# Kernel optimization log

Measured on AMD Instinct MI355X. Metric: run time of the kernel, lower is better.

## Reference

```python
import jax, jax.numpy as jnp
import numpy as np

G = 512        # graphs in batch
N_PER = 256    # nodes per graph (equal-size graphs)
D = 128        # embed_dim
E_PER = 4096   # edges per graph
KEEP = 0.5
K = int(np.ceil(KEEP * N_PER))  # 128 nodes kept per graph (PyG topk: ceil(ratio*n))
N = G * N_PER
E = G * E_PER


def setup_inputs() -> dict:
    key = jax.random.key(0)
    k1, k2, k3, k4, k5 = jax.random.split(key, 5)
    x = jax.random.normal(k1, (N, D), jnp.float32)
    offs = (jnp.arange(G, dtype=jnp.int32) * N_PER)[:, None]
    src = jax.random.randint(k2, (G, E_PER), 0, N_PER, dtype=jnp.int32) + offs
    dst = jax.random.randint(k3, (G, E_PER), 0, N_PER, dtype=jnp.int32) + offs
    edge_index = jnp.stack([src.reshape(-1), dst.reshape(-1)], axis=0)  # [2, E], within-graph edges
    graph_indicator = jnp.repeat(jnp.arange(G, dtype=jnp.int32), N_PER)  # [N]
    gcn_w = jax.random.normal(k4, (D, 1), jnp.float32) / np.sqrt(D)
    gcn_b = jnp.zeros((1,), jnp.float32)
    lin_w = jax.random.normal(k5, (2 * D, D), jnp.float32) / np.sqrt(2 * D)
    lin_b = jnp.zeros((D,), jnp.float32)
    return {"input_feature": x, "graph_indicator": graph_indicator, "edge_index": edge_index,
            "gcn_w": gcn_w, "gcn_b": gcn_b, "lin_w": lin_w, "lin_b": lin_b}


def gcn_conv(x, edge_index, w, b):
    # PyG GCNConv: add self-loops, symmetric normalization, aggregate at target (edge_index[1]).
    n = x.shape[0]
    loop = jnp.arange(n, dtype=edge_index.dtype)
    row = jnp.concatenate([edge_index[0], loop])  # source
    col = jnp.concatenate([edge_index[1], loop])  # target
    deg = jax.ops.segment_sum(jnp.ones_like(col, dtype=x.dtype), col, num_segments=n)
    dinv = jax.lax.rsqrt(deg)  # deg >= 1 due to self-loops
    norm = dinv[row] * dinv[col]            # [E+N]
    xw = x @ w                              # [N, out]
    msg = xw[row] * norm[:, None]           # gather + scale
    agg = jax.ops.segment_sum(msg, col, num_segments=n)
    return agg + b


def reference(input_feature, graph_indicator, edge_index, gcn_w, gcn_b, lin_w, lin_b):
    # SAGPool: attention scores via GCNConv(d -> 1)
    score = gcn_conv(input_feature, edge_index, gcn_w, gcn_b).squeeze(-1)  # [N]
    # per-graph top-k mask (equal-size graphs -> reshape)
    s = score.reshape(G, N_PER)
    _, idx = jax.lax.top_k(s, K)                                          # [G, K]
    mask = jnp.zeros((G, N_PER), bool).at[jnp.arange(G)[:, None], idx].set(True)
    # gated features of kept nodes: x[mask] * tanh(score[mask])
    feat = (input_feature * jnp.tanh(score)[:, None]).reshape(G, N_PER, D)
    m = mask[..., None]
    # global mean/max pool over kept nodes per graph (exactly K kept per graph)
    mean = jnp.sum(jnp.where(m, feat, 0.0), axis=1) / K                   # [G, D]
    mx = jnp.max(jnp.where(m, feat, -jnp.inf), axis=1)                    # [G, D]
    readout = jnp.concatenate([mean, mx], axis=1)                         # [G, 2D]
    return readout @ lin_w + lin_b                                        # [G, D]
```

## Files before the change

kernel.cpp:

```cpp
#include <hip/hip_runtime.h>
#include <math.h>

#define NG   512
#define NPER 256
#define DD   128
#define EPER 4096
#define KK   128
#define NT   1024
#define NW   16

#define SFX_SCALE 4194304.0f
#define SFX_INV   2.384185791015625e-07f

#define BAR() asm volatile("s_waitcnt lgkmcnt(0)\ns_barrier" ::: "memory")

__global__ __launch_bounds__(NT, 8) void sag_fused(
    const float* __restrict__ x,
    const int*   __restrict__ esrc,
    const int*   __restrict__ edst,
    const float* __restrict__ gcn_w,
    const float* __restrict__ gcn_b,
    const float* __restrict__ lin_w,
    const float* __restrict__ lin_b,
    float* __restrict__ out)
{
  const int g    = blockIdx.x;
  const int tid  = threadIdx.x;
  const int lane = tid & 63;
  const int wave = tid >> 6;
  const int j    = lane & 15;
  const int sub  = lane >> 4;
  const int slot = wave * 4 + sub;

  __shared__ int    sDeg[NPER];
  __shared__ int    sRank[NPER];
  __shared__ int    sXWi[NPER];
  __shared__ __align__(16) int   sFx[NPER];
  __shared__ float  sXW[NPER];
  __shared__ float  sDinv[NPER];
  __shared__ __align__(16) float sScore[NPER];
  __shared__ float2 sGF[NPER];
  __shared__ float  sPoolS[NW][DD];
  __shared__ float  sPoolM[NW][DD];
  __shared__ float2 sR2[DD];
  float* sR = (float*)sR2;

  const int4* es4 = (const int4*)(esrc + (size_t)g * EPER);
  const int4* ed4 = (const int4*)(edst + (size_t)g * EPER);
  int4 da = ed4[tid];
  int4 sa = es4[tid];

  float4 wa = ((const float4*)gcn_w)[j];
  float4 wb = ((const float4*)gcn_w)[16 + j];

  const float4* xg4 = (const float4*)(x + (size_t)g * NPER * DD);
  const int colbase = slot * 32 + j;
  float4 q0[4], q1[4];
  #pragma unroll
  for (int r = 0; r < 4; ++r) {
    q0[r] = xg4[r * 2048 + colbase];
    q1[r] = xg4[r * 2048 + colbase + 16];
  }

  if (tid < NPER) { sDeg[tid] = 1; sRank[tid] = 0; }
  BAR();

  atomicAdd(&sDeg[da.x & 255], 1);
  atomicAdd(&sDeg[da.y & 255], 1);
  atomicAdd(&sDeg[da.z & 255], 1);
  atomicAdd(&sDeg[da.w & 255], 1);

  #pragma unroll
  for (int r = 0; r < 4; ++r) {
    float acc = q0[r].x*wa.x + q0[r].y*wa.y + q0[r].z*wa.z + q0[r].w*wa.w
              + q1[r].x*wb.x + q1[r].y*wb.y + q1[r].z*wb.z + q1[r].w*wb.w;
    acc += __shfl_xor(acc, 1);
    acc += __shfl_xor(acc, 2);
    acc += __shfl_xor(acc, 4);
    acc += __shfl_xor(acc, 8);
    if (j == 0) sXW[r * 64 + slot] = acc;
  }
  BAR();

  if (tid < NPER) {
    float dv = 1.0f / sqrtf((float)sDeg[tid]);
    int   xi = __float2int_rn(sXW[tid] * dv * SFX_SCALE);
    sDinv[tid] = dv;
    sXWi[tid]  = xi;
    sFx[tid]   = xi;
  }
  BAR();

  {
    int v0 = sXWi[sa.x & 255];
    int v1 = sXWi[sa.y & 255];
    int v2 = sXWi[sa.z & 255];
    int v3 = sXWi[sa.w & 255];
    atomicAdd(&sFx[da.x & 255], v0);
    atomicAdd(&sFx[da.y & 255], v1);
    atomicAdd(&sFx[da.z & 255], v2);
    atomicAdd(&sFx[da.w & 255], v3);
  }
  BAR();

  if (tid < NPER) sScore[tid] = sDinv[tid] * ((float)sFx[tid] * SFX_INV);
  BAR();

  {
    const float4* sScore4 = (const float4*)sScore;
    int node = tid & 255;
    int seg  = tid >> 8;
    float s_i = sScore[node];
    int base = seg * 16;
    int part = 0;
    #pragma unroll 8
    for (int t = 0; t < 16; ++t) {
      float4 v = sScore4[base + t];
      int jj = (base + t) * 4;
      part += (v.x > s_i) || (v.x == s_i && (jj + 0) < node);
      part += (v.y > s_i) || (v.y == s_i && (jj + 1) < node);
      part += (v.z > s_i) || (v.z == s_i && (jj + 2) < node);
      part += (v.w > s_i) || (v.w == s_i && (jj + 3) < node);
    }
    atomicAdd(&sRank[node], part);
  }
  BAR();

  if (tid < NPER) {
    bool kp = sRank[tid] < KK;
    float gate = tanhf(sScore[tid] + gcn_b[0]);
    sGF[tid] = make_float2(kp ? gate : 0.0f, kp ? 0.0f : INFINITY);
  }
  BAR();

  float su0=0,su1=0,su2=0,su3=0,su4=0,su5=0,su6=0,su7=0;
  float mx0=-INFINITY,mx1=-INFINITY,mx2=-INFINITY,mx3=-INFINITY;
  float mx4=-INFINITY,mx5=-INFINITY,mx6=-INFINITY,mx7=-INFINITY;
  #pragma unroll
  for (int r = 0; r < 4; ++r) {
    float2 gf = sGF[r * 64 + slot];
    float g1 = gf.x, fb = gf.y;
    float a;
    a = q0[r].x * g1; su0 += a; mx0 = fmaxf(mx0, a - fb);
    a = q0[r].y * g1; su1 += a; mx1 = fmaxf(mx1, a - fb);
    a = q0[r].z * g1; su2 += a; mx2 = fmaxf(mx2, a - fb);
    a = q0[r].w * g1; su3 += a; mx3 = fmaxf(mx3, a - fb);
    a = q1[r].x * g1; su4 += a; mx4 = fmaxf(mx4, a - fb);
    a = q1[r].y * g1; su5 += a; mx5 = fmaxf(mx5, a - fb);
    a = q1[r].z * g1; su6 += a; mx6 = fmaxf(mx6, a - fb);
    a = q1[r].w * g1; su7 += a; mx7 = fmaxf(mx7, a - fb);
  }
  #define RED_S(v) v += __shfl_xor(v,16); v += __shfl_xor(v,32);
  #define RED_M(v) v = fmaxf(v,__shfl_xor(v,16)); v = fmaxf(v,__shfl_xor(v,32));
  RED_S(su0) RED_S(su1) RED_S(su2) RED_S(su3)
  RED_S(su4) RED_S(su5) RED_S(su6) RED_S(su7)
  RED_M(mx0) RED_M(mx1) RED_M(mx2) RED_M(mx3)
  RED_M(mx4) RED_M(mx5) RED_M(mx6) RED_M(mx7)
  if (sub == 0) {
    ((float4*)&sPoolS[wave][4 * j])[0]      = make_float4(su0, su1, su2, su3);
    ((float4*)&sPoolS[wave][64 + 4 * j])[0] = make_float4(su4, su5, su6, su7);
    ((float4*)&sPoolM[wave][4 * j])[0]      = make_float4(mx0, mx1, mx2, mx3);
    ((float4*)&sPoolM[wave][64 + 4 * j])[0] = make_float4(mx4, mx5, mx6, mx7);
  }
  BAR();

  if (tid < DD) {
    float s = 0.f;
    #pragma unroll
    for (int w = 0; w < NW; ++w) s += sPoolS[w][tid];
    sR[tid] = s * (1.0f / KK);
  } else if (tid < 2 * DD) {
    int d = tid - DD;
    float m = -INFINITY;
    #pragma unroll
    for (int w = 0; w < NW; ++w) m = fmaxf(m, sPoolM[w][d]);
    sR[tid] = m;
  }
  BAR();

  const float2* lw2 = (const float2*)lin_w;
  float a0 = 0.f, a1 = 0.f;
  #pragma unroll
  for (int t = 0; t < 8; ++t) {
    int k2 = wave * 8 + t;
    float2 rv = sR2[k2];
    float2 p0 = lw2[(2 * k2) * 64 + lane];
    float2 p1 = lw2[(2 * k2 + 1) * 64 + lane];
    a0 += rv.x * p0.x + rv.y * p1.x;
    a1 += rv.x * p0.y + rv.y * p1.y;
  }
  float2* sP2 = (float2*)sPoolS;
  sP2[wave * 64 + lane] = make_float2(a0, a1);
  BAR();
  if (wave == 0) {
    float2 a = sP2[lane];
    #pragma unroll
    for (int w = 1; w < NW; ++w) { float2 p = sP2[w * 64 + lane]; a.x += p.x; a.y += p.y; }
    float2 bb = ((const float2*)lin_b)[lane];
    a.x += bb.x; a.y += bb.y;
    ((float2*)out)[(size_t)g * 64 + lane] = a;
  }
}

extern "C" void kernel_launch(void* const* d_in, const int* in_sizes, int n_in,
                              void* d_out, int out_size, void* d_ws, size_t ws_size,
                              hipStream_t stream) {
  const float* x  = (const float*)d_in[0];
  const int*   ei = (const int*)d_in[2];
  const float* gw = (const float*)d_in[3];
  const float* gb = (const float*)d_in[4];
  const float* lw = (const float*)d_in[5];
  const float* lb = (const float*)d_in[6];
  float* out = (float*)d_out;
  const int E = in_sizes[2] / 2;
  sag_fused<<<NG, NT, 0, stream>>>(x, ei, ei + E, gw, gb, lw, lb, out);
}
```

Before: 119.0 us.

## Process two graphs per workgroup and re-read node features for pooling

Each 1024-thread block now handles two graphs, doubling per-block shared-memory arrays and the register-held edge and feature tiles, and the grid shrinks to half as many blocks. The features are loaded once for the score matvec and loaded again from global memory (likely L2-resident) for the pooling phase, so the first copy does not have to stay live across all the barriers. The aim is to amortise the barrier chain and the lin_w reads over two graphs and give each thread more independent memory work. The costs are more registers per thread, lower occupancy (launch bounds drop to 4), half as many blocks to fill the GPU, and a second read of x.

```diff
diff --git a/kernel.cpp b/kernel.cpp
--- a/kernel.cpp
+++ b/kernel.cpp
@@ -7,14 +7,13 @@
 #define EPER 4096
 #define KK   128
 #define NT   1024
-#define NW   16
 
 #define SFX_SCALE 4194304.0f
 #define SFX_INV   2.384185791015625e-07f
 
 #define BAR() asm volatile("s_waitcnt lgkmcnt(0)\ns_barrier" ::: "memory")
 
-__global__ __launch_bounds__(NT, 8) void sag_fused(
+__global__ __launch_bounds__(NT, 4) void sag_fused2(
     const float* __restrict__ x,
     const int*   __restrict__ esrc,
     const int*   __restrict__ edst,
@@ -24,7 +23,8 @@
     const float* __restrict__ lin_b,
     float* __restrict__ out)
 {
-  const int g    = blockIdx.x;
+  const int g0   = blockIdx.x * 2;
+  const int g1x  = g0 + 1;
   const int tid  = threadIdx.x;
   const int lane = tid & 63;
   const int wave = tid >> 6;
@@ -32,173 +32,204 @@
   const int sub  = lane >> 4;
   const int slot = wave * 4 + sub;
 
-  __shared__ int    sDeg[NPER];
-  __shared__ int    sRank[NPER];
-  __shared__ int    sXWi[NPER];
-  __shared__ __align__(16) int   sFx[NPER];
-  __shared__ float  sXW[NPER];
-  __shared__ float  sDinv[NPER];
-  __shared__ __align__(16) float sScore[NPER];
-  __shared__ float2 sGF[NPER];
-  __shared__ float  sPoolS[NW][DD];
-  __shared__ float  sPoolM[NW][DD];
-  __shared__ float2 sR2[DD];
-  float* sR = (float*)sR2;
-
-  const int4* es4 = (const int4*)(esrc + (size_t)g * EPER);
-  const int4* ed4 = (const int4*)(edst + (size_t)g * EPER);
-  int4 da = ed4[tid];
-  int4 sa = es4[tid];
+  __shared__ int    sDeg [2][NPER];
+  __shared__ int    sRank[2][NPER];
+  __shared__ int    sXWi [2][NPER];
+  __shared__ __align__(16) int   sFx[2][NPER];
+  __shared__ float  sXW  [2][NPER];
+  __shared__ float  sDinv[2][NPER];
+  __shared__ __align__(16) float sScore[2][NPER];
+  __shared__ float2 sGF  [2][NPER];
+  __shared__ float  sPoolS[2][16][DD];
+  __shared__ float  sPoolM[2][16][DD];
+  __shared__ float2 sR2  [2][DD];
+
+  const int4* es0 = (const int4*)(esrc + (size_t)g0  * EPER);
+  const int4* ed0 = (const int4*)(edst + (size_t)g0  * EPER);
+  const int4* es1 = (const int4*)(esrc + (size_t)g1x * EPER);
+  const int4* ed1 = (const int4*)(edst + (size_t)g1x * EPER);
+  int4 da0 = ed0[tid], da1 = ed1[tid];
+  int4 sa0 = es0[tid], sa1 = es1[tid];
 
   float4 wa = ((const float4*)gcn_w)[j];
   float4 wb = ((const float4*)gcn_w)[16 + j];
 
-  const float4* xg4 = (const float4*)(x + (size_t)g * NPER * DD);
+  const float4* x0 = (const float4*)(x + (size_t)g0  * NPER * DD);
+  const float4* x1 = (const float4*)(x + (size_t)g1x * NPER * DD);
   const int colbase = slot * 32 + j;
-  float4 q0[4], q1[4];
+
+  float4 qa0[4], qb0[4], qa1[4], qb1[4];
   #pragma unroll
   for (int r = 0; r < 4; ++r) {
-    q0[r] = xg4[r * 2048 + colbase];
-    q1[r] = xg4[r * 2048 + colbase + 16];
-  }
-
-  if (tid < NPER) { sDeg[tid] = 1; sRank[tid] = 0; }
-  BAR();
-
-  atomicAdd(&sDeg[da.x & 255], 1);
-  atomicAdd(&sDeg[da.y & 255], 1);
-  atomicAdd(&sDeg[da.z & 255], 1);
-  atomicAdd(&sDeg[da.w & 255], 1);
+    qa0[r] = x0[r * 2048 + colbase];  qb0[r] = x0[r * 2048 + colbase + 16];
+    qa1[r] = x1[r * 2048 + colbase];  qb1[r] = x1[r * 2048 + colbase + 16];
+  }
+
+  if (tid < 2 * NPER) { ((int*)sDeg)[tid] = 1; ((int*)sRank)[tid] = 0; }
+  BAR();
+
+  atomicAdd(&sDeg[0][da0.x & 255], 1); atomicAdd(&sDeg[1][da1.x & 255], 1);
+  atomicAdd(&sDeg[0][da0.y & 255], 1); atomicAdd(&sDeg[1][da1.y & 255], 1);
+  atomicAdd(&sDeg[0][da0.z & 255], 1); atomicAdd(&sDeg[1][da1.z & 255], 1);
+  atomicAdd(&sDeg[0][da0.w & 255], 1); atomicAdd(&sDeg[1][da1.w & 255], 1);
 
   #pragma unroll
   for (int r = 0; r < 4; ++r) {
-    float acc = q0[r].x*wa.x + q0[r].y*wa.y + q0[r].z*wa.z + q0[r].w*wa.w
-              + q1[r].x*wb.x + q1[r].y*wb.y + q1[r].z*wb.z + q1[r].w*wb.w;
-    acc += __shfl_xor(acc, 1);
-    acc += __shfl_xor(acc, 2);
-    acc += __shfl_xor(acc, 4);
-    acc += __shfl_xor(acc, 8);
-    if (j == 0) sXW[r * 64 + slot] = acc;
-  }
-  BAR();
-
-  if (tid < NPER) {
-    float dv = 1.0f / sqrtf((float)sDeg[tid]);
-    int   xi = __float2int_rn(sXW[tid] * dv * SFX_SCALE);
-    sDinv[tid] = dv;
-    sXWi[tid]  = xi;
-    sFx[tid]   = xi;
+    float a0 = qa0[r].x*wa.x + qa0[r].y*wa.y + qa0[r].z*wa.z + qa0[r].w*wa.w
+             + qb0[r].x*wb.x + qb0[r].y*wb.y + qb0[r].z*wb.z + qb0[r].w*wb.w;
+    float a1 = qa1[r].x*wa.x + qa1[r].y*wa.y + qa1[r].z*wa.z + qa1[r].w*wa.w
+             + qb1[r].x*wb.x + qb1[r].y*wb.y + qb1[r].z*wb.z + qb1[r].w*wb.w;
+    a0 += __shfl_xor(a0, 1);  a1 += __shfl_xor(a1, 1);
+    a0 += __shfl_xor(a0, 2);  a1 += __shfl_xor(a1, 2);
+    a0 += __shfl_xor(a0, 4);  a1 += __shfl_xor(a1, 4);
+    a0 += __shfl_xor(a0, 8);  a1 += __shfl_xor(a1, 8);
+    if (j == 0) { sXW[0][r * 64 + slot] = a0; sXW[1][r * 64 + slot] = a1; }
+  }
+  BAR();
+
+  float4 ua0[4], ub0[4], ua1[4], ub1[4];
+  #pragma unroll
+  for (int r = 0; r < 4; ++r) {
+    ua0[r] = x0[r * 2048 + colbase];  ub0[r] = x0[r * 2048 + colbase + 16];
+    ua1[r] = x1[r * 2048 + colbase];  ub1[r] = x1[r * 2048 + colbase + 16];
+  }
+
+  if (tid < 2 * NPER) {
+    float dv = 1.0f / sqrtf((float)((int*)sDeg)[tid]);
+    int   xi = __float2int_rn(((float*)sXW)[tid] * dv * SFX_SCALE);
+    ((float*)sDinv)[tid] = dv;
+    ((int*)sXWi)[tid]    = xi;
+    ((int*)sFx)[tid]     = xi;
   }
   BAR();
 
   {
-    int v0 = sXWi[sa.x & 255];
-    int v1 = sXWi[sa.y & 255];
-    int v2 = sXWi[sa.z & 255];
-    int v3 = sXWi[sa.w & 255];
-    atomicAdd(&sFx[da.x & 255], v0);
-    atomicAdd(&sFx[da.y & 255], v1);
-    atomicAdd(&sFx[da.z & 255], v2);
-    atomicAdd(&sFx[da.w & 255], v3);
-  }
-  BAR();
-
-  if (tid < NPER) sScore[tid] = sDinv[tid] * ((float)sFx[tid] * SFX_INV);
+    int v0 = sXWi[0][sa0.x & 255], w0 = sXWi[1][sa1.x & 255];
+    int v1 = sXWi[0][sa0.y & 255], w1 = sXWi[1][sa1.y & 255];
+    int v2 = sXWi[0][sa0.z & 255], w2 = sXWi[1][sa1.z & 255];
+    int v3 = sXWi[0][sa0.w & 255], w3 = sXWi[1][sa1.w & 255];
+    atomicAdd(&sFx[0][da0.x & 255], v0); atomicAdd(&sFx[1][da1.x & 255], w0);
+    atomicAdd(&sFx[0][da0.y & 255], v1); atomicAdd(&sFx[1][da1.y & 255], w1);
+    atomicAdd(&sFx[0][da0.z & 255], v2); atomicAdd(&sFx[1][da1.z & 255], w2);
+    atomicAdd(&sFx[0][da0.w & 255], v3); atomicAdd(&sFx[1][da1.w & 255], w3);
+  }
+  BAR();
+
+  if (tid < 2 * NPER)
+    ((float*)sScore)[tid] = ((float*)sDinv)[tid] * ((float)((int*)sFx)[tid] * SFX_INV);
   BAR();
 
   {
-    const float4* sScore4 = (const float4*)sScore;
+    int G    = tid >> 9;
     int node = tid & 255;
-    int seg  = tid >> 8;
-    float s_i = sScore[node];
-    int base = seg * 16;
+    int seg  = (tid >> 8) & 1;
+    const float4* S4 = (const float4*)sScore[G];
+    float s_i = sScore[G][node];
+    int base = seg * 32;
     int part = 0;
     #pragma unroll 8
-    for (int t = 0; t < 16; ++t) {
-      float4 v = sScore4[base + t];
+    for (int t = 0; t < 32; ++t) {
+      float4 v = S4[base + t];
       int jj = (base + t) * 4;
       part += (v.x > s_i) || (v.x == s_i && (jj + 0) < node);
       part += (v.y > s_i) || (v.y == s_i && (jj + 1) < node);
       part += (v.z > s_i) || (v.z == s_i && (jj + 2) < node);
       part += (v.w > s_i) || (v.w == s_i && (jj + 3) < node);
     }
-    atomicAdd(&sRank[node], part);
-  }
-  BAR();
-
-  if (tid < NPER) {
-    bool kp = sRank[tid] < KK;
-    float gate = tanhf(sScore[tid] + gcn_b[0]);
-    sGF[tid] = make_float2(kp ? gate : 0.0f, kp ? 0.0f : INFINITY);
-  }
-  BAR();
-
-  float su0=0,su1=0,su2=0,su3=0,su4=0,su5=0,su6=0,su7=0;
-  float mx0=-INFINITY,mx1=-INFINITY,mx2=-INFINITY,mx3=-INFINITY;
-  float mx4=-INFINITY,mx5=-INFINITY,mx6=-INFINITY,mx7=-INFINITY;
-  #pragma unroll
-  for (int r = 0; r < 4; ++r) {
-    float2 gf = sGF[r * 64 + slot];
-    float g1 = gf.x, fb = gf.y;
-    float a;
-    a = q0[r].x * g1; su0 += a; mx0 = fmaxf(mx0, a - fb);
-    a = q0[r].y * g1; su1 += a; mx1 = fmaxf(mx1, a - fb);
-    a = q0[r].z * g1; su2 += a; mx2 = fmaxf(mx2, a - fb);
-    a = q0[r].w * g1; su3 += a; mx3 = fmaxf(mx3, a - fb);
-    a = q1[r].x * g1; su4 += a; mx4 = fmaxf(mx4, a - fb);
-    a = q1[r].y * g1; su5 += a; mx5 = fmaxf(mx5, a - fb);
-    a = q1[r].z * g1; su6 += a; mx6 = fmaxf(mx6, a - fb);
-    a = q1[r].w * g1; su7 += a; mx7 = fmaxf(mx7, a - fb);
-  }
+    atomicAdd(&sRank[G][node], part);
+  }
+  BAR();
+
+  if (tid < 2 * NPER) {
+    bool kp = ((int*)sRank)[tid] < KK;
+    float gate = tanhf(((float*)sScore)[tid] + gcn_b[0]);
+    ((float2*)sGF)[tid] = make_float2(kp ? gate : 0.0f, kp ? 0.0f : INFINITY);
+  }
+  BAR();
+
   #define RED_S(v) v += __shfl_xor(v,16); v += __shfl_xor(v,32);
   #define RED_M(v) v = fmaxf(v,__shfl_xor(v,16)); v = fmaxf(v,__shfl_xor(v,32));
-  RED_S(su0) RED_S(su1) RED_S(su2) RED_S(su3)
-  RED_S(su4) RED_S(su5) RED_S(su6) RED_S(su7)
-  RED_M(mx0) RED_M(mx1) RED_M(mx2) RED_M(mx3)
-  RED_M(mx4) RED_M(mx5) RED_M(mx6) RED_M(mx7)
-  if (sub == 0) {
-    ((float4*)&sPoolS[wave][4 * j])[0]      = make_float4(su0, su1, su2, su3);
-    ((float4*)&sPoolS[wave][64 + 4 * j])[0] = make_float4(su4, su5, su6, su7);
-    ((float4*)&sPoolM[wave][4 * j])[0]      = make_float4(mx0, mx1, mx2, mx3);
-    ((float4*)&sPoolM[wave][64 + 4 * j])[0] = make_float4(mx4, mx5, mx6, mx7);
-  }
-  BAR();
-
-  if (tid < DD) {
-    float s = 0.f;
+  #define POOL_ONE(G, UA, UB)                                               \
+  {                                                                         \
+    float su0=0,su1=0,su2=0,su3=0,su4=0,su5=0,su6=0,su7=0;                  \
+    float mx0=-INFINITY,mx1=-INFINITY,mx2=-INFINITY,mx3=-INFINITY;          \
+    float mx4=-INFINITY,mx5=-INFINITY,mx6=-INFINITY,mx7=-INFINITY;          \
+    _Pragma("unroll")                                                       \
+    for (int r = 0; r < 4; ++r) {                                           \
+      float2 gf = sGF[G][r * 64 + slot];                                    \
+      float gv = gf.x, fb = gf.y, a;                                        \
+      a = UA[r].x * gv; su0 += a; mx0 = fmaxf(mx0, a - fb);                 \
+      a = UA[r].y * gv; su1 += a; mx1 = fmaxf(mx1, a - fb);                 \
+      a = UA[r].z * gv; su2 += a; mx2 = fmaxf(mx2, a - fb);                 \
+      a = UA[r].w * gv; su3 += a; mx3 = fmaxf(mx3, a - fb);                 \
+      a = UB[r].x * gv; su4 += a; mx4 = fmaxf(mx4, a - fb);                 \
+      a = UB[r].y * gv; su5 += a; mx5 = fmaxf(mx5, a - fb);                 \
+      a = UB[r].z * gv; su6 += a; mx6 = fmaxf(mx6, a - fb);                 \
+      a = UB[r].w * gv; su7 += a; mx7 = fmaxf(mx7, a - fb);                 \
+    }                                                                       \
+    RED_S(su0) RED_S(su1) RED_S(su2) RED_S(su3)                             \
+    RED_S(su4) RED_S(su5) RED_S(su6) RED_S(su7)                             \
+    RED_M(mx0) RED_M(mx1) RED_M(mx2) RED_M(mx3)                             \
+    RED_M(mx4) RED_M(mx5) RED_M(mx6) RED_M(mx7)                             \
+    if (sub == 0) {                                                         \
+      ((float4*)&sPoolS[G][wave][4 * j])[0]      = make_float4(su0,su1,su2,su3); \
+      ((float4*)&sPoolS[G][wave][64 + 4 * j])[0] = make_float4(su4,su5,su6,su7); \
+      ((float4*)&sPoolM[G][wave][4 * j])[0]      = make_float4(mx0,mx1,mx2,mx3); \
+      ((float4*)&sPoolM[G][wave][64 + 4 * j])[0] = make_float4(mx4,mx5,mx6,mx7); \
+    }                                                                       \
+  }
+  POOL_ONE(0, ua0, ub0)
+  POOL_ONE(1, ua1, ub1)
+  BAR();
+
+  if (tid < 2 * NPER) {
+    int G = tid >> 8, idx = tid & 255;
+    float* sRf = (float*)sR2[G];
+    if (idx < DD) {
+      float s = 0.f;
+      #pragma unroll
+      for (int w = 0; w < 16; ++w) s += sPoolS[G][w][idx];
+      sRf[idx] = s * (1.0f / KK);
+    } else {
+      int d = idx - DD;
+      float m = -INFINITY;
+      #pragma unroll
+      for (int w = 0; w < 16; ++w) m = fmaxf(m, sPoolM[G][w][d]);
+      sRf[idx] = m;
+    }
+  }
+  BAR();
+
+  {
+    const float2* lw2 = (const float2*)lin_w;
+    int G  = wave >> 3;
+    int wg = wave & 7;
+    float a0 = 0.f, a1 = 0.f;
     #pragma unroll
-    for (int w = 0; w < NW; ++w) s += sPoolS[w][tid];
-    sR[tid] = s * (1.0f / KK);
-  } else if (tid < 2 * DD) {
-    int d = tid - DD;
-    float m = -INFINITY;
+    for (int t = 0; t < 16; ++t) {
+      int k2 = wg * 16 + t;
+      float2 rv = sR2[G][k2];
+      float2 p0 = lw2[(2 * k2) * 64 + lane];
+      float2 p1 = lw2[(2 * k2 + 1) * 64 + lane];
+      a0 += rv.x * p0.x + rv.y * p1.x;
+      a1 += rv.x * p0.y + rv.y * p1.y;
+    }
+    float2* sP2 = (float2*)sPoolS;
+    sP2[(G * 8 + wg) * 64 + lane] = make_float2(a0, a1);
+  }
+  BAR();
+  if ((wave & 7) == 0) {
+    int G = wave >> 3;
+    float2* sP2 = (float2*)sPoolS;
+    float2 a = sP2[G * 512 + lane];
     #pragma unroll
-    for (int w = 0; w < NW; ++w) m = fmaxf(m, sPoolM[w][d]);
-    sR[tid] = m;
-  }
-  BAR();
-
-  const float2* lw2 = (const float2*)lin_w;
-  float a0 = 0.f, a1 = 0.f;
-  #pragma unroll
-  for (int t = 0; t < 8; ++t) {
-    int k2 = wave * 8 + t;
-    float2 rv = sR2[k2];
-    float2 p0 = lw2[(2 * k2) * 64 + lane];
-    float2 p1 = lw2[(2 * k2 + 1) * 64 + lane];
-    a0 += rv.x * p0.x + rv.y * p1.x;
-    a1 += rv.x * p0.y + rv.y * p1.y;
-  }
-  float2* sP2 = (float2*)sPoolS;
-  sP2[wave * 64 + lane] = make_float2(a0, a1);
-  BAR();
-  if (wave == 0) {
-    float2 a = sP2[lane];
-    #pragma unroll
-    for (int w = 1; w < NW; ++w) { float2 p = sP2[w * 64 + lane]; a.x += p.x; a.y += p.y; }
+    for (int w = 1; w < 8; ++w) {
+      float2 p = sP2[G * 512 + w * 64 + lane];
+      a.x += p.x; a.y += p.y;
+    }
     float2 bb = ((const float2*)lin_b)[lane];
     a.x += bb.x; a.y += bb.y;
-    ((float2*)out)[(size_t)g * 64 + lane] = a;
+    ((float2*)out)[(size_t)(g0 + G) * 64 + lane] = a;
   }
 }
 
@@ -213,5 +244,5 @@
   const float* lb = (const float*)d_in[6];
   float* out = (float*)d_out;
   const int E = in_sizes[2] / 2;
-  sag_fused<<<NG, NT, 0, stream>>>(x, ei, ei + E, gw, gb, lw, lb, out);
+  sag_fused2<<<NG / 2, NT, 0, stream>>>(x, ei, ei + E, gw, gb, lw, lb, out);
 }
```

After: 130.9 us. 10.0% more time.

## Halve block size, split scatter accumulators, fuse pooled reduction via LDS atomics

Applied to the files above, without the earlier changes.

The block shrinks from 1024 to 512 threads, so each thread now handles two edge quads and eight node rows held in registers. The score scatter uses two lane-parity accumulator copies to reduce LDS atomic contention. Scores are no longer stored: they are recomputed from the fixed-point sums wherever needed. The per-wave pool partials are replaced by integer fixed-point atomicAdd for the sum and order-encoded atomicMax for the max. This cuts barriers and shared memory, but adds register pressure, extra recomputation in the rank loop, and fixed-point rounding of the mean.

```diff
diff --git a/kernel.cpp b/kernel.cpp
--- a/kernel.cpp
+++ b/kernel.cpp
@@ -6,15 +6,25 @@
 #define DD   128
 #define EPER 4096
 #define KK   128
-#define NT   1024
-#define NW   16
+#define NT   512
+#define NW   8
 
 #define SFX_SCALE 4194304.0f
 #define SFX_INV   2.384185791015625e-07f
+#define PSC_SCALE 1048576.0f
+#define PSC_INV   9.5367431640625e-07f
 
 #define BAR() asm volatile("s_waitcnt lgkmcnt(0)\ns_barrier" ::: "memory")
 
-__global__ __launch_bounds__(NT, 8) void sag_fused(
+__device__ __forceinline__ unsigned fenc(float f) {
+  unsigned u = __float_as_uint(f);
+  return (u & 0x80000000u) ? ~u : (u | 0x80000000u);
+}
+__device__ __forceinline__ float fdec(unsigned k) {
+  return __uint_as_float((k & 0x80000000u) ? (k ^ 0x80000000u) : ~k);
+}
+
+__global__ __launch_bounds__(NT, 4) void sag_fused(
     const float* __restrict__ x,
     const int*   __restrict__ esrc,
     const int*   __restrict__ edst,
@@ -32,53 +42,53 @@
   const int sub  = lane >> 4;
   const int slot = wave * 4 + sub;
 
-  __shared__ int    sDeg[NPER];
-  __shared__ int    sRank[NPER];
-  __shared__ int    sXWi[NPER];
-  __shared__ __align__(16) int   sFx[NPER];
-  __shared__ float  sXW[NPER];
-  __shared__ float  sDinv[NPER];
-  __shared__ __align__(16) float sScore[NPER];
-  __shared__ float2 sGF[NPER];
-  __shared__ float  sPoolS[NW][DD];
-  __shared__ float  sPoolM[NW][DD];
-  __shared__ float2 sR2[DD];
-  float* sR = (float*)sR2;
+  __shared__ int      sDeg[NPER];
+  __shared__ int      sRank[NPER];
+  __shared__ int      sXWi[NPER];
+  __shared__ __align__(16) int sFx[2][NPER];
+  __shared__ float    sXW[NPER];
+  __shared__ __align__(16) float sDinv[NPER];
+  __shared__ float2   sGF[NPER];
+  __shared__ int      sRm[DD];
+  __shared__ unsigned sRx[DD];
+  __shared__ float    sR[2 * DD];
+  __shared__ float2   sP2[NW * 64];
 
   const int4* es4 = (const int4*)(esrc + (size_t)g * EPER);
   const int4* ed4 = (const int4*)(edst + (size_t)g * EPER);
-  int4 da = ed4[tid];
-  int4 sa = es4[tid];
+  int4 da0 = ed4[tid], da1 = ed4[NT + tid];
+  int4 sa0 = es4[tid], sa1 = es4[NT + tid];
 
   float4 wa = ((const float4*)gcn_w)[j];
   float4 wb = ((const float4*)gcn_w)[16 + j];
 
   const float4* xg4 = (const float4*)(x + (size_t)g * NPER * DD);
   const int colbase = slot * 32 + j;
-  float4 q0[4], q1[4];
+  float4 q0[8], q1[8];
   #pragma unroll
-  for (int r = 0; r < 4; ++r) {
-    q0[r] = xg4[r * 2048 + colbase];
-    q1[r] = xg4[r * 2048 + colbase + 16];
-  }
-
-  if (tid < NPER) { sDeg[tid] = 1; sRank[tid] = 0; }
-  BAR();
-
-  atomicAdd(&sDeg[da.x & 255], 1);
-  atomicAdd(&sDeg[da.y & 255], 1);
-  atomicAdd(&sDeg[da.z & 255], 1);
-  atomicAdd(&sDeg[da.w & 255], 1);
+  for (int r = 0; r < 8; ++r) {
+    q0[r] = xg4[r * 1024 + colbase];
+    q1[r] = xg4[r * 1024 + colbase + 16];
+  }
+
+  if (tid < NPER)            { sDeg[tid] = 1; sRank[tid] = 0; }
+  else if (tid < NPER + DD)  { sRm[tid - NPER] = 0; sRx[tid - NPER] = 0u; }
+  BAR();
+
+  atomicAdd(&sDeg[da0.x & 255], 1); atomicAdd(&sDeg[da0.y & 255], 1);
+  atomicAdd(&sDeg[da0.z & 255], 1); atomicAdd(&sDeg[da0.w & 255], 1);
+  atomicAdd(&sDeg[da1.x & 255], 1); atomicAdd(&sDeg[da1.y & 255], 1);
+  atomicAdd(&sDeg[da1.z & 255], 1); atomicAdd(&sDeg[da1.w & 255], 1);
 
   #pragma unroll
-  for (int r = 0; r < 4; ++r) {
+  for (int r = 0; r < 8; ++r) {
     float acc = q0[r].x*wa.x + q0[r].y*wa.y + q0[r].z*wa.z + q0[r].w*wa.w
               + q1[r].x*wb.x + q1[r].y*wb.y + q1[r].z*wb.z + q1[r].w*wb.w;
     acc += __shfl_xor(acc, 1);
     acc += __shfl_xor(acc, 2);
     acc += __shfl_xor(acc, 4);
     acc += __shfl_xor(acc, 8);
-    if (j == 0) sXW[r * 64 + slot] = acc;
+    if (j == 0) sXW[r * 32 + slot] = acc;
   }
   BAR();
 
@@ -87,40 +97,51 @@
     int   xi = __float2int_rn(sXW[tid] * dv * SFX_SCALE);
     sDinv[tid] = dv;
     sXWi[tid]  = xi;
-    sFx[tid]   = xi;
+    sFx[0][tid] = xi;
+    sFx[1][tid] = 0;
   }
   BAR();
 
   {
-    int v0 = sXWi[sa.x & 255];
-    int v1 = sXWi[sa.y & 255];
-    int v2 = sXWi[sa.z & 255];
-    int v3 = sXWi[sa.w & 255];
-    atomicAdd(&sFx[da.x & 255], v0);
-    atomicAdd(&sFx[da.y & 255], v1);
-    atomicAdd(&sFx[da.z & 255], v2);
-    atomicAdd(&sFx[da.w & 255], v3);
-  }
-  BAR();
-
-  if (tid < NPER) sScore[tid] = sDinv[tid] * ((float)sFx[tid] * SFX_INV);
+    int p = lane & 1;
+    int v0 = sXWi[sa0.x & 255], v1 = sXWi[sa0.y & 255];
+    int v2 = sXWi[sa0.z & 255], v3 = sXWi[sa0.w & 255];
+    int v4 = sXWi[sa1.x & 255], v5 = sXWi[sa1.y & 255];
+    int v6 = sXWi[sa1.z & 255], v7 = sXWi[sa1.w & 255];
+    atomicAdd(&sFx[p][da0.x & 255], v0);
+    atomicAdd(&sFx[p][da0.y & 255], v1);
+    atomicAdd(&sFx[p][da0.z & 255], v2);
+    atomicAdd(&sFx[p][da0.w & 255], v3);
+    atomicAdd(&sFx[p][da1.x & 255], v4);
+    atomicAdd(&sFx[p][da1.y & 255], v5);
+    atomicAdd(&sFx[p][da1.z & 255], v6);
+    atomicAdd(&sFx[p][da1.w & 255], v7);
+  }
   BAR();
 
   {
-    const float4* sScore4 = (const float4*)sScore;
+    const int4*   c04 = (const int4*)sFx[0];
+    const int4*   c14 = (const int4*)sFx[1];
+    const float4* dv4 = (const float4*)sDinv;
     int node = tid & 255;
     int seg  = tid >> 8;
-    float s_i = sScore[node];
-    int base = seg * 16;
+    float s_i = sDinv[node] * ((float)(sFx[0][node] + sFx[1][node]) * SFX_INV);
+    int base = seg * 32;
     int part = 0;
     #pragma unroll 8
-    for (int t = 0; t < 16; ++t) {
-      float4 v = sScore4[base + t];
+    for (int t = 0; t < 32; ++t) {
+      int4   c0 = c04[base + t];
+      int4   c1 = c14[base + t];
+      float4 dv = dv4[base + t];
+      float vx = dv.x * ((float)(c0.x + c1.x) * SFX_INV);
+      float vy = dv.y * ((float)(c0.y + c1.y) * SFX_INV);
+      float vz = dv.z * ((float)(c0.z + c1.z) * SFX_INV);
+      float vw = dv.w * ((float)(c0.w + c1.w) * SFX_INV);
       int jj = (base + t) * 4;
-      part += (v.x > s_i) || (v.x == s_i && (jj + 0) < node);
-      part += (v.y > s_i) || (v.y == s_i && (jj + 1) < node);
-      part += (v.z > s_i) || (v.z == s_i && (jj + 2) < node);
-      part += (v.w > s_i) || (v.w == s_i && (jj + 3) < node);
+      part += (vx > s_i) || (vx == s_i && (jj + 0) < node);
+      part += (vy > s_i) || (vy == s_i && (jj + 1) < node);
+      part += (vz > s_i) || (vz == s_i && (jj + 2) < node);
+      part += (vw > s_i) || (vw == s_i && (jj + 3) < node);
     }
     atomicAdd(&sRank[node], part);
   }
@@ -128,7 +149,8 @@
 
   if (tid < NPER) {
     bool kp = sRank[tid] < KK;
-    float gate = tanhf(sScore[tid] + gcn_b[0]);
+    float sc = sDinv[tid] * ((float)(sFx[0][tid] + sFx[1][tid]) * SFX_INV);
+    float gate = tanhf(sc + gcn_b[0]);
     sGF[tid] = make_float2(kp ? gate : 0.0f, kp ? 0.0f : INFINITY);
   }
   BAR();
@@ -137,8 +159,8 @@
   float mx0=-INFINITY,mx1=-INFINITY,mx2=-INFINITY,mx3=-INFINITY;
   float mx4=-INFINITY,mx5=-INFINITY,mx6=-INFINITY,mx7=-INFINITY;
   #pragma unroll
-  for (int r = 0; r < 4; ++r) {
-    float2 gf = sGF[r * 64 + slot];
+  for (int r = 0; r < 8; ++r) {
+    float2 gf = sGF[r * 32 + slot];
     float g1 = gf.x, fb = gf.y;
     float a;
     a = q0[r].x * g1; su0 += a; mx0 = fmaxf(mx0, a - fb);
@@ -157,40 +179,45 @@
   RED_M(mx0) RED_M(mx1) RED_M(mx2) RED_M(mx3)
   RED_M(mx4) RED_M(mx5) RED_M(mx6) RED_M(mx7)
   if (sub == 0) {
-    ((float4*)&sPoolS[wave][4 * j])[0]      = make_float4(su0, su1, su2, su3);
-    ((float4*)&sPoolS[wave][64 + 4 * j])[0] = make_float4(su4, su5, su6, su7);
-    ((float4*)&sPoolM[wave][4 * j])[0]      = make_float4(mx0, mx1, mx2, mx3);
-    ((float4*)&sPoolM[wave][64 + 4 * j])[0] = make_float4(mx4, mx5, mx6, mx7);
-  }
-  BAR();
-
-  if (tid < DD) {
-    float s = 0.f;
+    int d0 = 4 * j, d1 = 64 + 4 * j;
+    atomicAdd(&sRm[d0 + 0], __float2int_rn(su0 * PSC_SCALE));
+    atomicAdd(&sRm[d0 + 1], __float2int_rn(su1 * PSC_SCALE));
+    atomicAdd(&sRm[d0 + 2], __float2int_rn(su2 * PSC_SCALE));
+    atomicAdd(&sRm[d0 + 3], __float2int_rn(su3 * PSC_SCALE));
+    atomicAdd(&sRm[d1 + 0], __float2int_rn(su4 * PSC_SCALE));
+    atomicAdd(&sRm[d1 + 1], __float2int_rn(su5 * PSC_SCALE));
+    atomicAdd(&sRm[d1 + 2], __float2int_rn(su6 * PSC_SCALE));
+    atomicAdd(&sRm[d1 + 3], __float2int_rn(su7 * PSC_SCALE));
+    atomicMax(&sRx[d0 + 0], fenc(mx0));
+    atomicMax(&sRx[d0 + 1], fenc(mx1));
+    atomicMax(&sRx[d0 + 2], fenc(mx2));
+    atomicMax(&sRx[d0 + 3], fenc(mx3));
+    atomicMax(&sRx[d1 + 0], fenc(mx4));
+    atomicMax(&sRx[d1 + 1], fenc(mx5));
+    atomicMax(&sRx[d1 + 2], fenc(mx6));
+    atomicMax(&sRx[d1 + 3], fenc(mx7));
+  }
+  BAR();
+
+  if (tid < DD)          sR[tid] = (float)sRm[tid] * (PSC_INV / (float)KK);
+  else if (tid < 2 * DD) sR[tid] = fdec(sRx[tid - DD]);
+  BAR();
+
+  {
+    const float2* lw2 = (const float2*)lin_w;
+    const float2* sR2 = (const float2*)sR;
+    float a0 = 0.f, a1 = 0.f;
     #pragma unroll
-    for (int w = 0; w < NW; ++w) s += sPoolS[w][tid];
-    sR[tid] = s * (1.0f / KK);
-  } else if (tid < 2 * DD) {
-    int d = tid - DD;
-    float m = -INFINITY;
-    #pragma unroll
-    for (int w = 0; w < NW; ++w) m = fmaxf(m, sPoolM[w][d]);
-    sR[tid] = m;
-  }
-  BAR();
-
-  const float2* lw2 = (const float2*)lin_w;
-  float a0 = 0.f, a1 = 0.f;
-  #pragma unroll
-  for (int t = 0; t < 8; ++t) {
-    int k2 = wave * 8 + t;
-    float2 rv = sR2[k2];
-    float2 p0 = lw2[(2 * k2) * 64 + lane];
-    float2 p1 = lw2[(2 * k2 + 1) * 64 + lane];
-    a0 += rv.x * p0.x + rv.y * p1.x;
-    a1 += rv.x * p0.y + rv.y * p1.y;
-  }
-  float2* sP2 = (float2*)sPoolS;
-  sP2[wave * 64 + lane] = make_float2(a0, a1);
+    for (int t = 0; t < 16; ++t) {
+      int k2 = wave * 16 + t;
+      float2 rv = sR2[k2];
+      float2 p0 = lw2[(2 * k2) * 64 + lane];
+      float2 p1 = lw2[(2 * k2 + 1) * 64 + lane];
+      a0 += rv.x * p0.x + rv.y * p1.x;
+      a1 += rv.x * p0.y + rv.y * p1.y;
+    }
+    sP2[wave * 64 + lane] = make_float2(a0, a1);
+  }
   BAR();
   if (wave == 0) {
     float2 a = sP2[lane];
```

Result: slower. 122.7 us (+3.1%).
